# Performance work log

Measured on AMD Instinct MI355X. Metric: run time of the kernel, lower is better.

## Reference

```python
import jax, jax.numpy as jnp
import numpy as np
from jax import lax

D_MODEL = 1024
D_STATE = 16
EXPAND = 2
KERNEL = 4
BATCH = 4
SEQ = 4096
LN_EPS = 1e-5


def _ln(x, w, b):
    m = jnp.mean(x, axis=-1, keepdims=True)
    v = jnp.mean((x - m) ** 2, axis=-1, keepdims=True)
    return (x - m) * lax.rsqrt(v + LN_EPS) * w + b


def setup_inputs() -> dict:
    key = jax.random.key(0)
    ks = jax.random.split(key, 16)
    d, n, e, k = D_MODEL, D_STATE, EXPAND, KERNEL

    def lin(key, fan_in, shape):
        bound = 1.0 / np.sqrt(fan_in)
        return jax.random.uniform(key, shape, jnp.float32, -bound, bound)

    return {
        "x": jax.random.normal(ks[0], (BATCH, SEQ, d), jnp.float32),
        "ln1_w": jnp.ones((d,), jnp.float32),
        "ln1_b": jnp.zeros((d,), jnp.float32),
        "conv_w": lin(ks[1], k, (d, 1, k)),  # depthwise conv, groups=d -> fan_in=k
        "conv_b": lin(ks[2], k, (d,)),
        "lns_w": jnp.ones((d,), jnp.float32),
        "lns_b": jnp.zeros((d,), jnp.float32),
        "in_w": lin(ks[3], d, (d, 2 * d)),
        "in_b": lin(ks[4], d, (2 * d,)),
        "xp_w": lin(ks[5], d, (d, n)),
        "xp_b": lin(ks[6], d, (n,)),
        "A_log": jax.random.normal(ks[7], (n,), jnp.float32),
        "D": jax.random.normal(ks[8], (n, d), jnp.float32),
        "out_w": lin(ks[9], d, (d, d)),
        "out_b": lin(ks[10], d, (d,)),
        "ln2_w": jnp.ones((d,), jnp.float32),
        "ln2_b": jnp.zeros((d,), jnp.float32),
        "mlp_w1": lin(ks[11], d, (d, e * d)),
        "mlp_b1": lin(ks[12], d, (e * d,)),
        "mlp_w2": lin(ks[13], e * d, (e * d, d)),
        "mlp_b2": lin(ks[14], e * d, (d,)),
    }


def reference(x, ln1_w, ln1_b, conv_w, conv_b, lns_w, lns_b, in_w, in_b,
              xp_w, xp_b, A_log, D, out_w, out_b, ln2_w, ln2_b,
              mlp_w1, mlp_b1, mlp_w2, mlp_b2):
    b, s, d = x.shape
    # --- depthwise causal-padded conv branch (truncated to seq_len) ---
    xn = _ln(x, ln1_w, ln1_b)
    xc = jnp.transpose(xn, (0, 2, 1))  # (b, d, s)
    xc = lax.conv_general_dilated(
        xc, conv_w, window_strides=(1,), padding=[(KERNEL - 1, KERNEL - 1)],
        feature_group_count=d, dimension_numbers=("NCH", "OIH", "NCH"))
    xc = xc + conv_b[None, :, None]
    xc = jnp.transpose(xc, (0, 2, 1))[:, :s]  # (b, s, d)
    x = x + xc

    # --- SelectiveScanLayer ---
    residual = x
    xn = _ln(x, lns_w, lns_b)
    xz = xn @ in_w + in_b
    xp, z = jnp.split(xz, 2, axis=-1)
    xp = jax.nn.silu(xp)
    z = jax.nn.sigmoid(z)
    u = xp @ xp_w + xp_b  # (b, s, n)
    decay = jnp.exp(-jnp.exp(A_log))  # exp(A), A = -exp(A_log); (n,)

    u_t = jnp.transpose(u, (1, 0, 2))  # (s, b, n)

    def step(h, u_i):
        h = decay * h + u_i
        return h, h

    _, hs = lax.scan(step, jnp.zeros((b, D_STATE), x.dtype), u_t)  # (s, b, n)
    ys = jnp.einsum("sbn,nd->sbd", hs, D) * jnp.transpose(z, (1, 0, 2))
    ys = ys @ out_w + out_b  # (s, b, d)
    # faithful to original: torch stack gives (1,s,b,d), then .view(b,s,d)
    y = ys.reshape(b, s, d)
    x = residual + y

    # --- MLP (dropout inactive at eval) ---
    h = _ln(x, ln2_w, ln2_b)
    h = jax.nn.gelu(h @ mlp_w1 + mlp_b1, approximate=False)
    h = h @ mlp_w2 + mlp_b2
    return x + h
```

## Files before the change

### kernel.cpp

```cpp
#include <hip/hip_runtime.h>
#include <cstdint>
#include <cstddef>


typedef short bf16x8 __attribute__((ext_vector_type(8)));
typedef float f32x4 __attribute__((ext_vector_type(4)));

#define GLD16(gp, lp)                                                          \
  __builtin_amdgcn_global_load_lds(                                            \
      (__attribute__((address_space(1))) void*)(gp),                           \
      (__attribute__((address_space(3))) void*)(lp), 16, 0, 0)

static __device__ __forceinline__ ushort f2bf(float f) {
  union { float f; uint32_t u; } c; c.f = f;
  uint32_t r = c.u + 0x7FFFu + ((c.u >> 16) & 1u);
  return (ushort)(r >> 16);
}
static __device__ __forceinline__ float bf2f(ushort u) {
  union { uint32_t u; float f; } c; c.u = ((uint32_t)u) << 16;
  return c.f;
}

template <int BF16OUT>
__global__ __launch_bounds__(256) void ln_kernel(
    const float* __restrict__ x, const float* __restrict__ w,
    const float* __restrict__ b, void* __restrict__ out) {
  const int row = blockIdx.x;
  const int tid = threadIdx.x;
  const float4 v = ((const float4*)(x + (size_t)row * 1024))[tid];
  float s  = v.x + v.y + v.z + v.w;
  float s2 = v.x * v.x + v.y * v.y + v.z * v.z + v.w * v.w;
#pragma unroll
  for (int off = 32; off > 0; off >>= 1) {
    s  += __shfl_down(s, off);
    s2 += __shfl_down(s2, off);
  }
  __shared__ float red[8];
  const int wv = tid >> 6, ln = tid & 63;
  if (ln == 0) { red[wv] = s; red[4 + wv] = s2; }
  __syncthreads();
  s  = red[0] + red[1] + red[2] + red[3];
  s2 = red[4] + red[5] + red[6] + red[7];
  const float mean = s * (1.f / 1024.f);
  const float var  = s2 * (1.f / 1024.f) - mean * mean;
  const float rstd = rsqrtf(var + 1e-5f);
  const float4 wv4 = ((const float4*)w)[tid];
  const float4 bv4 = ((const float4*)b)[tid];
  const float o0 = (v.x - mean) * rstd * wv4.x + bv4.x;
  const float o1 = (v.y - mean) * rstd * wv4.y + bv4.y;
  const float o2 = (v.z - mean) * rstd * wv4.z + bv4.z;
  const float o3 = (v.w - mean) * rstd * wv4.w + bv4.w;
  if (BF16OUT) {
    ushort4 o; o.x = f2bf(o0); o.y = f2bf(o1); o.z = f2bf(o2); o.w = f2bf(o3);
    ((ushort4*)((ushort*)out + (size_t)row * 1024))[tid] = o;
  } else {
    float4 o; o.x = o0; o.y = o1; o.z = o2; o.w = o3;
    ((float4*)((float*)out + (size_t)row * 1024))[tid] = o;
  }
}

__global__ __launch_bounds__(256) void lnconv_kernel(
    const float* __restrict__ x, const float* __restrict__ ln1w,
    const float* __restrict__ ln1b, const float* __restrict__ cw,
    const float* __restrict__ cb, const float* __restrict__ lnsw,
    const float* __restrict__ lnsb, float* __restrict__ x1,
    ushort* __restrict__ abuf) {
  const int row = blockIdx.x;
  const int t = row & 4095;
  const int tid = threadIdx.x;
  const int wv = tid >> 6, ln = tid & 63;
  const float4* x4 = (const float4*)x;
  float4 xr[4];
  float s[4], q[4];
#pragma unroll
  for (int j = 0; j < 4; j++) {
    const int tt = t - 3 + j;
    if (tt >= 0)
      xr[j] = x4[(size_t)(row - 3 + j) * 256 + tid];
    else
      xr[j] = make_float4(0.f, 0.f, 0.f, 0.f);
    s[j] = xr[j].x + xr[j].y + xr[j].z + xr[j].w;
    q[j] = xr[j].x * xr[j].x + xr[j].y * xr[j].y + xr[j].z * xr[j].z +
           xr[j].w * xr[j].w;
  }
#pragma unroll
  for (int off = 32; off > 0; off >>= 1) {
#pragma unroll
    for (int j = 0; j < 4; j++) {
      s[j] += __shfl_down(s[j], off);
      q[j] += __shfl_down(q[j], off);
    }
  }
  __shared__ float red[4][8];
  __shared__ float red2[8];
  if (ln == 0) {
#pragma unroll
    for (int j = 0; j < 4; j++) { red[wv][j] = s[j]; red[wv][4 + j] = q[j]; }
  }
  __syncthreads();
  float4 wv4 = ((const float4*)ln1w)[tid];
  float4 bv4 = ((const float4*)ln1b)[tid];
  const int c0 = tid * 4;
  float4 acc = *(const float4*)(cb + c0);
  const float4 w0 = *(const float4*)(cw + (size_t)(c0 + 0) * 4);
  const float4 w1 = *(const float4*)(cw + (size_t)(c0 + 1) * 4);
  const float4 w2 = *(const float4*)(cw + (size_t)(c0 + 2) * 4);
  const float4 w3 = *(const float4*)(cw + (size_t)(c0 + 3) * 4);
#pragma unroll
  for (int j = 0; j < 4; j++) {
    if (t - 3 + j >= 0) {
      const float sm = red[0][j] + red[1][j] + red[2][j] + red[3][j];
      const float sq = red[0][4 + j] + red[1][4 + j] + red[2][4 + j] +
                       red[3][4 + j];
      const float mean = sm * (1.f / 1024.f);
      const float var  = sq * (1.f / 1024.f) - mean * mean;
      const float rstd = rsqrtf(var + 1e-5f);
      const float lx = (xr[j].x - mean) * rstd * wv4.x + bv4.x;
      const float ly = (xr[j].y - mean) * rstd * wv4.y + bv4.y;
      const float lz = (xr[j].z - mean) * rstd * wv4.z + bv4.z;
      const float lw = (xr[j].w - mean) * rstd * wv4.w + bv4.w;
      acc.x += lx * ((const float*)&w0)[j];
      acc.y += ly * ((const float*)&w1)[j];
      acc.z += lz * ((const float*)&w2)[j];
      acc.w += lw * ((const float*)&w3)[j];
    }
  }
  float4 o;
  o.x = xr[3].x + acc.x; o.y = xr[3].y + acc.y;
  o.z = xr[3].z + acc.z; o.w = xr[3].w + acc.w;
  ((float4*)x1)[(size_t)row * 256 + tid] = o;
  float s2 = o.x + o.y + o.z + o.w;
  float q2 = o.x * o.x + o.y * o.y + o.z * o.z + o.w * o.w;
#pragma unroll
  for (int off = 32; off > 0; off >>= 1) {
    s2 += __shfl_down(s2, off);
    q2 += __shfl_down(q2, off);
  }
  if (ln == 0) { red2[wv] = s2; red2[4 + wv] = q2; }
  __syncthreads();
  const float sm = red2[0] + red2[1] + red2[2] + red2[3];
  const float sq = red2[4] + red2[5] + red2[6] + red2[7];
  const float mean = sm * (1.f / 1024.f);
  const float var  = sq * (1.f / 1024.f) - mean * mean;
  const float rstd = rsqrtf(var + 1e-5f);
  wv4 = ((const float4*)lnsw)[tid];
  bv4 = ((const float4*)lnsb)[tid];
  ushort4 a;
  a.x = f2bf((o.x - mean) * rstd * wv4.x + bv4.x);
  a.y = f2bf((o.y - mean) * rstd * wv4.y + bv4.y);
  a.z = f2bf((o.z - mean) * rstd * wv4.z + bv4.z);
  a.w = f2bf((o.w - mean) * rstd * wv4.w + bv4.w);
  ((ushort4*)(abuf + (size_t)row * 1024))[tid] = a;
}

__global__ __launch_bounds__(256) void wt_all_kernel(
    const float* __restrict__ in_w, const float* __restrict__ out_w,
    const float* __restrict__ w1, const float* __restrict__ w2,
    ushort* __restrict__ in_wT, ushort* __restrict__ out_wT,
    ushort* __restrict__ w1T, ushort* __restrict__ w2T) {
  __shared__ float tile[32][33];
  const int idx = blockIdx.x;
  const float* src; ushort* dst; int K, N, n0, k0;
  if (idx < 2048) {
    src = in_w; dst = in_wT; K = 1024; N = 2048;
    n0 = (idx & 63) * 32; k0 = (idx >> 6) * 32;
  } else if (idx < 3072) {
    const int r = idx - 2048;
    src = out_w; dst = out_wT; K = 1024; N = 1024;
    n0 = (r & 31) * 32; k0 = (r >> 5) * 32;
  } else if (idx < 5120) {
    const int r = idx - 3072;
    src = w1; dst = w1T; K = 1024; N = 2048;
    n0 = (r & 63) * 32; k0 = (r >> 6) * 32;
  } else {
    const int r = idx - 5120;
    src = w2; dst = w2T; K = 2048; N = 1024;
    n0 = (r & 31) * 32; k0 = (r >> 5) * 32;
  }
  const int tx = threadIdx.x & 31, ty = threadIdx.x >> 5;
#pragma unroll
  for (int j = 0; j < 32; j += 8)
    tile[ty + j][tx] = src[(size_t)(k0 + ty + j) * N + n0 + tx];
  __syncthreads();
#pragma unroll
  for (int j = 0; j < 32; j += 8)
    dst[(size_t)(n0 + ty + j) * K + k0 + tx] = f2bf(tile[tx][ty + j]);
}

__global__ __launch_bounds__(256) void u_mfma_kernel(
    const ushort* __restrict__ xp, const float* __restrict__ xpw,
    const float* __restrict__ xpb, float* __restrict__ u) {
  __shared__ ushort Ws[16 * 1024];
  __shared__ ushort As[64 * 64];
  const int tid = threadIdx.x;
  const int wave = tid >> 6, lane = tid & 63;
  const int l16 = lane & 15, quad = lane >> 4;
  for (int e = tid; e < 16384; e += 256) {
    const int n = e & 15, k = e >> 4;
    Ws[n * 1024 + (((k >> 3) ^ (n & 7)) << 3) + (k & 7)] =
        f2bf(xpw[(size_t)k * 16 + n]);
  }
  const int bm0 = blockIdx.x * 64;
  const int srow = lane >> 3, sblk = (lane & 7) ^ (srow & 7);
  const ushort* Ag = xp + (size_t)(bm0 + wave * 16 + srow) * 1024 + sblk * 8;
  ushort* Al = &As[wave * 16 * 64];
  const int rsw = l16 & 7;
  f32x4 acc = (f32x4){0.f, 0.f, 0.f, 0.f};
  __syncthreads();
  for (int k0 = 0; k0 < 1024; k0 += 64) {
    GLD16(Ag + k0, Al);
    GLD16(Ag + k0 + (size_t)8 * 1024, Al + 512);
    __syncthreads();
#pragma unroll
    for (int kh = 0; kh < 2; kh++) {
      const bf16x8 aF = *(const bf16x8*)
          &As[(wave * 16 + l16) * 64 + (((kh * 4 + quad) ^ rsw) << 3)];
      const bf16x8 bF = *(const bf16x8*)
          &Ws[l16 * 1024 + ((((k0 >> 3) + kh * 4 + quad) ^ rsw) << 3)];
      acc = __builtin_amdgcn_mfma_f32_16x16x32_bf16(aF, bF, acc, 0, 0, 0);
    }
    __syncthreads();
  }
  const float bv = xpb[l16];
#pragma unroll
  for (int r = 0; r < 4; r++) {
    const int row = bm0 + wave * 16 + quad * 4 + r;
    u[(size_t)row * 16 + l16] = acc[r] + bv;
  }
}

__global__ __launch_bounds__(256) void scan_kernel(
    const float* __restrict__ u, const float* __restrict__ A_log,
    float* __restrict__ hs) {
  const int tid = threadIdx.x;
  const int b = blockIdx.x >> 4;
  const int n = blockIdx.x & 15;
  const float d = expf(-expf(A_log[n]));
  const int t0 = tid * 16;
  const float* up = u + ((size_t)b * 4096) * 16 + n;
  float loc[16];
  float h = 0.f;
#pragma unroll
  for (int i = 0; i < 16; i++) {
    h = d * h + up[(size_t)(t0 + i) * 16];
    loc[i] = h;
  }
  __shared__ float sv[256];
  sv[tid] = h;
  __syncthreads();
  float d16 = d * d; d16 *= d16; d16 *= d16; d16 *= d16;
  float f = d16;
  for (int off = 1; off < 256; off <<= 1) {
    const float add = (tid >= off) ? sv[tid - off] : 0.f;
    __syncthreads();
    sv[tid] += f * add;
    __syncthreads();
    f *= f;
  }
  const float carry = (tid > 0) ? sv[tid - 1] : 0.f;
  float dp = d;
#pragma unroll
  for (int i = 0; i < 16; i++) {
    const float hg = loc[i] + dp * carry;
    dp *= d;
    hs[((size_t)(t0 + i) * 4 + b) * 16 + n] = hg;
  }
}

__global__ __launch_bounds__(256) void g_kernel(
    const float* __restrict__ hs, const float* __restrict__ Dm,
    const ushort* __restrict__ z, ushort* __restrict__ g) {
  __shared__ float hsh[256];
  const int tid = threadIdx.x;
  const int r0 = blockIdx.x * 16;
  hsh[tid] = hs[(size_t)r0 * 16 + tid];
  __syncthreads();
  float4 acc[16];
#pragma unroll
  for (int rr = 0; rr < 16; rr++) acc[rr] = make_float4(0.f, 0.f, 0.f, 0.f);
  const float4* Dv = (const float4*)Dm;
#pragma unroll
  for (int n = 0; n < 16; n++) {
    const float4 dv = Dv[(size_t)n * 256 + tid];
#pragma unroll
    for (int rr = 0; rr < 16; rr++) {
      const float h = hsh[rr * 16 + n];
      acc[rr].x += h * dv.x; acc[rr].y += h * dv.y;
      acc[rr].z += h * dv.z; acc[rr].w += h * dv.w;
    }
  }
#pragma unroll
  for (int rr = 0; rr < 16; rr++) {
    const int r = r0 + rr;
    const int b = r & 3, t = r >> 2;
    const ushort4 zv =
        *(const ushort4*)(z + ((size_t)b * 4096 + t) * 1024 + tid * 4);
    ushort4 o;
    o.x = f2bf(acc[rr].x * bf2f(zv.x)); o.y = f2bf(acc[rr].y * bf2f(zv.y));
    o.z = f2bf(acc[rr].z * bf2f(zv.z)); o.w = f2bf(acc[rr].w * bf2f(zv.w));
    *(ushort4*)(g + (size_t)r * 1024 + tid * 4) = o;
  }
}

template <int EPI>
__global__ __launch_bounds__(512, 2) void gemm_bt(
    const ushort* __restrict__ A, const ushort* __restrict__ Bt,
    const float* __restrict__ bias, int K, void* __restrict__ p0,
    void* __restrict__ p1) {
  __shared__ __align__(16) ushort sm[65536];
  const int tid = threadIdx.x;
  const int wave = tid >> 6, lane = tid & 63;
  const int l16 = lane & 15, quad = lane >> 4;
  const int wm = wave >> 2, wn = wave & 3;

  const int nbx = (int)gridDim.x;
  int tm, tn;
  if ((nbx & 7) == 0) {
    const int lid = (int)blockIdx.y * nbx + (int)blockIdx.x;
    const int ncm = nbx >> 3;
    const int xcd = lid & 7;
    const int j = lid >> 3;
    tm = xcd * ncm + (j % ncm);
    tn = j / ncm;
  } else {
    tm = (int)blockIdx.x; tn = (int)blockIdx.y;
  }
  const int bm0 = tm * 256, bn0 = tn * 256;

  const int srow = lane >> 3;
  const int sblk = (lane & 7) ^ srow;
  const int NT = K >> 6;

  const ushort* Astg = A + (size_t)(bm0 + wave * 8 + srow) * K + sblk * 8;
  const ushort* Bstg = Bt + (size_t)(bn0 + wave * 8 + srow) * K + sblk * 8;

#define SA(i, kt, base)                                                        \
  GLD16(Astg + (size_t)((i) * 64) * K + (kt) * 64,                             \
        &sm[(base) + (i) * 4096 + wave * 512])
#define SB(i, kt, base)                                                        \
  GLD16(Bstg + (size_t)((i) * 64) * K + (kt) * 64,                             \
        &sm[(base) + 16384 + (i) * 4096 + wave * 512])

  const int rsw = l16 & 7;
  const int c80 = (quad ^ rsw) << 3;
  const int c81 = ((4 + quad) ^ rsw) << 3;
  const int aoff = (wm * 128 + l16) * 64;
  const int boff = 16384 + (wn * 64 + l16) * 64;

  f32x4 acc[8][4];
#pragma unroll
  for (int i = 0; i < 8; i++)
#pragma unroll
    for (int j = 0; j < 4; j++) acc[i][j] = (f32x4){0.f, 0.f, 0.f, 0.f};

  SA(0, 0, 0); SA(1, 0, 0); SA(2, 0, 0); SA(3, 0, 0);
  SB(0, 0, 0); SB(1, 0, 0); SB(2, 0, 0); SB(3, 0, 0);
  if (NT > 1) {
    SA(0, 1, 32768); SA(1, 1, 32768);
    asm volatile("s_waitcnt vmcnt(2)" ::: "memory");
  } else {
    asm volatile("s_waitcnt vmcnt(0)" ::: "memory");
  }
  __builtin_amdgcn_s_barrier();

  bf16x8 af[4][2], b01[2][2], b23[2][2];

  for (int t = 0; t < NT; ++t) {
    const int cb = (t & 1) << 15;
    const int nb = cb ^ 32768;
#pragma unroll
    for (int i = 0; i < 4; i++) {
      af[i][0] = *(const bf16x8*)&sm[cb + aoff + i * 1024 + c80];
      af[i][1] = *(const bf16x8*)&sm[cb + aoff + i * 1024 + c81];
    }
#pragma unroll
    for (int j = 0; j < 2; j++) {
      b01[j][0] = *(const bf16x8*)&sm[cb + boff + j * 1024 + c80];
      b01[j][1] = *(const bf16x8*)&sm[cb + boff + j * 1024 + c81];
    }
    if (t + 1 < NT) { SA(2, t + 1, nb); SA(3, t + 1, nb); }
    __builtin_amdgcn_s_barrier();
    asm volatile("s_waitcnt lgkmcnt(0)" ::: "memory");
    __builtin_amdgcn_sched_barrier(0);
    __builtin_amdgcn_s_setprio(1);
#pragma unroll
    for (int i = 0; i < 4; i++)
#pragma unroll
      for (int j = 0; j < 2; j++) {
        acc[i][j] = __builtin_amdgcn_mfma_f32_16x16x32_bf16(
            af[i][0], b01[j][0], acc[i][j], 0, 0, 0);
        acc[i][j] = __builtin_amdgcn_mfma_f32_16x16x32_bf16(
            af[i][1], b01[j][1], acc[i][j], 0, 0, 0);
      }
    __builtin_amdgcn_s_setprio(0);
    __builtin_amdgcn_s_barrier();
#pragma unroll
    for (int j = 0; j < 2; j++) {
      b23[j][0] = *(const bf16x8*)&sm[cb + boff + (2 + j) * 1024 + c80];
      b23[j][1] = *(const bf16x8*)&sm[cb + boff + (2 + j) * 1024 + c81];
    }
    if (t + 1 < NT) { SB(0, t + 1, nb); SB(1, t + 1, nb); }
    __builtin_amdgcn_s_barrier();
    asm volatile("s_waitcnt lgkmcnt(0)" ::: "memory");
    __builtin_amdgcn_sched_barrier(0);
    __builtin_amdgcn_s_setprio(1);
#pragma unroll
    for (int i = 0; i < 4; i++)
#pragma unroll
      for (int j = 0; j < 2; j++) {
        acc[i][2 + j] = __builtin_amdgcn_mfma_f32_16x16x32_bf16(
            af[i][0], b23[j][0], acc[i][2 + j], 0, 0, 0);
        acc[i][2 + j] = __builtin_amdgcn_mfma_f32_16x16x32_bf16(
            af[i][1], b23[j][1], acc[i][2 + j], 0, 0, 0);
      }
    __builtin_amdgcn_s_setprio(0);
    __builtin_amdgcn_s_barrier();
#pragma unroll
    for (int i = 0; i < 4; i++) {
      af[i][0] = *(const bf16x8*)&sm[cb + aoff + (4 + i) * 1024 + c80];
      af[i][1] = *(const bf16x8*)&sm[cb + aoff + (4 + i) * 1024 + c81];
    }
    if (t + 1 < NT) { SB(2, t + 1, nb); SB(3, t + 1, nb); }
    __builtin_amdgcn_s_barrier();
    asm volatile("s_waitcnt lgkmcnt(0)" ::: "memory");
    __builtin_amdgcn_sched_barrier(0);
    __builtin_amdgcn_s_setprio(1);
#pragma unroll
    for (int i = 0; i < 4; i++)
#pragma unroll
      for (int j = 0; j < 2; j++) {
        acc[4 + i][j] = __builtin_amdgcn_mfma_f32_16x16x32_bf16(
            af[i][0], b01[j][0], acc[4 + i][j], 0, 0, 0);
        acc[4 + i][j] = __builtin_amdgcn_mfma_f32_16x16x32_bf16(
            af[i][1], b01[j][1], acc[4 + i][j], 0, 0, 0);
      }
    __builtin_amdgcn_s_setprio(0);
    __builtin_amdgcn_s_barrier();
    if (t + 2 < NT) { SA(0, t + 2, cb); SA(1, t + 2, cb); }
    __builtin_amdgcn_s_barrier();
    __builtin_amdgcn_s_setprio(1);
#pragma unroll
    for (int i = 0; i < 4; i++)
#pragma unroll
      for (int j = 0; j < 2; j++) {
        acc[4 + i][2 + j] = __builtin_amdgcn_mfma_f32_16x16x32_bf16(
            af[i][0], b23[j][0], acc[4 + i][2 + j], 0, 0, 0);
        acc[4 + i][2 + j] = __builtin_amdgcn_mfma_f32_16x16x32_bf16(
            af[i][1], b23[j][1], acc[4 + i][2 + j], 0, 0, 0);
      }
    __builtin_amdgcn_s_setprio(0);
    if (t + 2 < NT) {
      asm volatile("s_waitcnt vmcnt(2)" ::: "memory");
    } else {
      asm volatile("s_waitcnt vmcnt(0)" ::: "memory");
    }
    __builtin_amdgcn_s_barrier();
  }
#undef SA
#undef SB

#pragma unroll
  for (int i = 0; i < 8; i++) {
    const int row0 = bm0 + wm * 128 + i * 16 + quad * 4;
#pragma unroll
    for (int j = 0; j < 4; j++) {
      const int c = bn0 + wn * 64 + j * 16 + l16;
      const float bv = bias[c];
#pragma unroll
      for (int r = 0; r < 4; r++) {
        const size_t row = (size_t)(row0 + r);
        const float v = acc[i][j][r] + bv;
        if (EPI == 0) {
          if (c < 1024)
            ((ushort*)p0)[row * 1024 + c] = f2bf(v / (1.f + __expf(-v)));
          else
            ((ushort*)p1)[row * 1024 + (c - 1024)] =
                f2bf(1.f / (1.f + __expf(-v)));
        } else if (EPI == 1) {
          float* io = (float*)p0;
          io[row * 1024 + c] += v;
        } else if (EPI == 2) {
          ((ushort*)p0)[row * 2048 + c] =
              f2bf(0.5f * v * (1.f + erff(v * 0.70710678118654752f)));
        } else {
          ((float*)p0)[row * 1024 + c] =
              ((const float*)p1)[row * 1024 + c] + v;
        }
      }
    }
  }
}

extern "C" void kernel_launch(void* const* d_in, const int* in_sizes, int n_in,
                              void* d_out, int out_size, void* d_ws,
                              size_t ws_size, hipStream_t stream) {
  const float* x      = (const float*)d_in[0];
  const float* ln1_w  = (const float*)d_in[1];
  const float* ln1_b  = (const float*)d_in[2];
  const float* conv_w = (const float*)d_in[3];
  const float* conv_b = (const float*)d_in[4];
  const float* lns_w  = (const float*)d_in[5];
  const float* lns_b  = (const float*)d_in[6];
  const float* in_w   = (const float*)d_in[7];
  const float* in_b   = (const float*)d_in[8];
  const float* xp_w   = (const float*)d_in[9];
  const float* xp_b   = (const float*)d_in[10];
  const float* A_log  = (const float*)d_in[11];
  const float* Dm     = (const float*)d_in[12];
  const float* out_w  = (const float*)d_in[13];
  const float* out_b  = (const float*)d_in[14];
  const float* ln2_w  = (const float*)d_in[15];
  const float* ln2_b  = (const float*)d_in[16];
  const float* mlp_w1 = (const float*)d_in[17];
  const float* mlp_b1 = (const float*)d_in[18];
  const float* mlp_w2 = (const float*)d_in[19];
  const float* mlp_b2 = (const float*)d_in[20];

  char* wsp = (char*)d_ws;
  size_t off = 0;
  auto alloc = [&](size_t bytes) {
    void* p = wsp + off;
    off += (bytes + 255) & ~(size_t)255;
    return p;
  };
  float*  x1    = (float*)alloc(67108864);
  ushort* abuf  = (ushort*)alloc(67108864);
  ushort* gbuf  = abuf + 16777216;
  ushort* xpb   = (ushort*)alloc(33554432);
  ushort* zb    = (ushort*)alloc(67108864);
  ushort* h1b   = (ushort*)zb;
  float*  ub    = (float*)alloc(1048576);
  float*  hsb   = (float*)alloc(1048576);
  ushort* in_wT = (ushort*)alloc(4194304);
  ushort* out_wT= (ushort*)alloc(2097152);
  ushort* w1T   = (ushort*)alloc(4194304);
  ushort* w2T   = (ushort*)alloc(4194304);

  wt_all_kernel<<<7168, 256, 0, stream>>>(in_w, out_w, mlp_w1, mlp_w2,
                                          in_wT, out_wT, w1T, w2T);
  lnconv_kernel<<<16384, 256, 0, stream>>>(x, ln1_w, ln1_b, conv_w, conv_b,
                                           lns_w, lns_b, x1, abuf);
  gemm_bt<0><<<dim3(64, 8), 512, 0, stream>>>(abuf, in_wT, in_b, 1024,
                                              xpb, zb);
  u_mfma_kernel<<<256, 256, 0, stream>>>(xpb, xp_w, xp_b, ub);
  scan_kernel<<<64, 256, 0, stream>>>(ub, A_log, hsb);
  g_kernel<<<1024, 256, 0, stream>>>(hsb, Dm, zb, gbuf);
  gemm_bt<1><<<dim3(64, 4), 512, 0, stream>>>(gbuf, out_wT, out_b, 1024,
                                              x1, nullptr);
  ln_kernel<1><<<16384, 256, 0, stream>>>(x1, ln2_w, ln2_b, xpb);
  gemm_bt<2><<<dim3(64, 8), 512, 0, stream>>>(xpb, w1T, mlp_b1, 1024,
                                              h1b, nullptr);
  gemm_bt<3><<<dim3(64, 4), 512, 0, stream>>>(h1b, w2T, mlp_b2, 2048,
                                              d_out, x1);
}
```

Measured before the change: 618.9 us.

## Prefetch whole next tiles up front and vectorize GEMM epilogue via transposed MFMA

The GEMM main loop no longer interleaves partial prefetches of the next K-tile between compute phases. It now issues all A and B loads for tile t+2 in one batch and waits with vmcnt(8), and one barrier is removed. The MFMA operand order is swapped so each lane holds four consecutive output columns. That lets the epilogue use float4 bias loads and 4-wide bf16 or float stores instead of scalar strided stores. The risk is that clustered loads cut overlap with compute and put more pressure on the double buffer's timing.

```diff
diff --git a/kernel.cpp b/kernel.cpp
--- a/kernel.cpp
+++ b/kernel.cpp
@@ -353,11 +353,12 @@
 #pragma unroll
     for (int j = 0; j < 4; j++) acc[i][j] = (f32x4){0.f, 0.f, 0.f, 0.f};
 
-  SA(0, 0, 0); SA(1, 0, 0); SA(2, 0, 0); SA(3, 0, 0);
-  SB(0, 0, 0); SB(1, 0, 0); SB(2, 0, 0); SB(3, 0, 0);
+#pragma unroll
+  for (int i = 0; i < 4; i++) { SA(i, 0, 0); SB(i, 0, 0); }
   if (NT > 1) {
-    SA(0, 1, 32768); SA(1, 1, 32768);
-    asm volatile("s_waitcnt vmcnt(2)" ::: "memory");
+#pragma unroll
+    for (int i = 0; i < 4; i++) { SA(i, 1, 32768); SB(i, 1, 32768); }
+    asm volatile("s_waitcnt vmcnt(8)" ::: "memory");
   } else {
     asm volatile("s_waitcnt vmcnt(0)" ::: "memory");
   }
@@ -367,7 +368,6 @@
 
   for (int t = 0; t < NT; ++t) {
     const int cb = (t & 1) << 15;
-    const int nb = cb ^ 32768;
 #pragma unroll
     for (int i = 0; i < 4; i++) {
       af[i][0] = *(const bf16x8*)&sm[cb + aoff + i * 1024 + c80];
@@ -378,7 +378,6 @@
       b01[j][0] = *(const bf16x8*)&sm[cb + boff + j * 1024 + c80];
       b01[j][1] = *(const bf16x8*)&sm[cb + boff + j * 1024 + c81];
     }
-    if (t + 1 < NT) { SA(2, t + 1, nb); SA(3, t + 1, nb); }
     __builtin_amdgcn_s_barrier();
     asm volatile("s_waitcnt lgkmcnt(0)" ::: "memory");
     __builtin_amdgcn_sched_barrier(0);
@@ -388,9 +387,9 @@
 #pragma unroll
       for (int j = 0; j < 2; j++) {
         acc[i][j] = __builtin_amdgcn_mfma_f32_16x16x32_bf16(
-            af[i][0], b01[j][0], acc[i][j], 0, 0, 0);
+            b01[j][0], af[i][0], acc[i][j], 0, 0, 0);
         acc[i][j] = __builtin_amdgcn_mfma_f32_16x16x32_bf16(
-            af[i][1], b01[j][1], acc[i][j], 0, 0, 0);
+            b01[j][1], af[i][1], acc[i][j], 0, 0, 0);
       }
     __builtin_amdgcn_s_setprio(0);
     __builtin_amdgcn_s_barrier();
@@ -399,7 +398,6 @@
       b23[j][0] = *(const bf16x8*)&sm[cb + boff + (2 + j) * 1024 + c80];
       b23[j][1] = *(const bf16x8*)&sm[cb + boff + (2 + j) * 1024 + c81];
     }
-    if (t + 1 < NT) { SB(0, t + 1, nb); SB(1, t + 1, nb); }
     __builtin_amdgcn_s_barrier();
     asm volatile("s_waitcnt lgkmcnt(0)" ::: "memory");
     __builtin_amdgcn_sched_barrier(0);
@@ -409,9 +407,9 @@
 #pragma unroll
       for (int j = 0; j < 2; j++) {
         acc[i][2 + j] = __builtin_amdgcn_mfma_f32_16x16x32_bf16(
-            af[i][0], b23[j][0], acc[i][2 + j], 0, 0, 0);
+            b23[j][0], af[i][0], acc[i][2 + j], 0, 0, 0);
         acc[i][2 + j] = __builtin_amdgcn_mfma_f32_16x16x32_bf16(
-            af[i][1], b23[j][1], acc[i][2 + j], 0, 0, 0);
+            b23[j][1], af[i][1], acc[i][2 + j], 0, 0, 0);
       }
     __builtin_amdgcn_s_setprio(0);
     __builtin_amdgcn_s_barrier();
@@ -420,7 +418,6 @@
       af[i][0] = *(const bf16x8*)&sm[cb + aoff + (4 + i) * 1024 + c80];
       af[i][1] = *(const bf16x8*)&sm[cb + aoff + (4 + i) * 1024 + c81];
     }
-    if (t + 1 < NT) { SB(2, t + 1, nb); SB(3, t + 1, nb); }
     __builtin_amdgcn_s_barrier();
     asm volatile("s_waitcnt lgkmcnt(0)" ::: "memory");
     __builtin_amdgcn_sched_barrier(0);
@@ -430,27 +427,29 @@
 #pragma unroll
       for (int j = 0; j < 2; j++) {
         acc[4 + i][j] = __builtin_amdgcn_mfma_f32_16x16x32_bf16(
-            af[i][0], b01[j][0], acc[4 + i][j], 0, 0, 0);
+            b01[j][0], af[i][0], acc[4 + i][j], 0, 0, 0);
         acc[4 + i][j] = __builtin_amdgcn_mfma_f32_16x16x32_bf16(
-            af[i][1], b01[j][1], acc[4 + i][j], 0, 0, 0);
+            b01[j][1], af[i][1], acc[4 + i][j], 0, 0, 0);
       }
     __builtin_amdgcn_s_setprio(0);
     __builtin_amdgcn_s_barrier();
-    if (t + 2 < NT) { SA(0, t + 2, cb); SA(1, t + 2, cb); }
-    __builtin_amdgcn_s_barrier();
+    if (t + 2 < NT) {
+#pragma unroll
+      for (int i = 0; i < 4; i++) { SA(i, t + 2, cb); SB(i, t + 2, cb); }
+    }
     __builtin_amdgcn_s_setprio(1);
 #pragma unroll
     for (int i = 0; i < 4; i++)
 #pragma unroll
       for (int j = 0; j < 2; j++) {
         acc[4 + i][2 + j] = __builtin_amdgcn_mfma_f32_16x16x32_bf16(
-            af[i][0], b23[j][0], acc[4 + i][2 + j], 0, 0, 0);
+            b23[j][0], af[i][0], acc[4 + i][2 + j], 0, 0, 0);
         acc[4 + i][2 + j] = __builtin_amdgcn_mfma_f32_16x16x32_bf16(
-            af[i][1], b23[j][1], acc[4 + i][2 + j], 0, 0, 0);
+            b23[j][1], af[i][1], acc[4 + i][2 + j], 0, 0, 0);
       }
     __builtin_amdgcn_s_setprio(0);
     if (t + 2 < NT) {
-      asm volatile("s_waitcnt vmcnt(2)" ::: "memory");
+      asm volatile("s_waitcnt vmcnt(8)" ::: "memory");
     } else {
       asm volatile("s_waitcnt vmcnt(0)" ::: "memory");
     }
@@ -461,31 +460,48 @@
 
 #pragma unroll
   for (int i = 0; i < 8; i++) {
-    const int row0 = bm0 + wm * 128 + i * 16 + quad * 4;
+    const size_t row = (size_t)(bm0 + wm * 128 + i * 16 + l16);
 #pragma unroll
     for (int j = 0; j < 4; j++) {
-      const int c = bn0 + wn * 64 + j * 16 + l16;
-      const float bv = bias[c];
-#pragma unroll
-      for (int r = 0; r < 4; r++) {
-        const size_t row = (size_t)(row0 + r);
-        const float v = acc[i][j][r] + bv;
-        if (EPI == 0) {
-          if (c < 1024)
-            ((ushort*)p0)[row * 1024 + c] = f2bf(v / (1.f + __expf(-v)));
-          else
-            ((ushort*)p1)[row * 1024 + (c - 1024)] =
-                f2bf(1.f / (1.f + __expf(-v)));
-        } else if (EPI == 1) {
-          float* io = (float*)p0;
-          io[row * 1024 + c] += v;
-        } else if (EPI == 2) {
-          ((ushort*)p0)[row * 2048 + c] =
-              f2bf(0.5f * v * (1.f + erff(v * 0.70710678118654752f)));
+      const int c = bn0 + wn * 64 + j * 16 + quad * 4;
+      const float4 bv = *(const float4*)(bias + c);
+      const float v0 = acc[i][j][0] + bv.x;
+      const float v1 = acc[i][j][1] + bv.y;
+      const float v2 = acc[i][j][2] + bv.z;
+      const float v3 = acc[i][j][3] + bv.w;
+      if (EPI == 0) {
+        ushort4 o;
+        if (c < 1024) {
+          o.x = f2bf(v0 / (1.f + __expf(-v0)));
+          o.y = f2bf(v1 / (1.f + __expf(-v1)));
+          o.z = f2bf(v2 / (1.f + __expf(-v2)));
+          o.w = f2bf(v3 / (1.f + __expf(-v3)));
+          *(ushort4*)((ushort*)p0 + row * 1024 + c) = o;
         } else {
-          ((float*)p0)[row * 1024 + c] =
-              ((const float*)p1)[row * 1024 + c] + v;
+          o.x = f2bf(1.f / (1.f + __expf(-v0)));
+          o.y = f2bf(1.f / (1.f + __expf(-v1)));
+          o.z = f2bf(1.f / (1.f + __expf(-v2)));
+          o.w = f2bf(1.f / (1.f + __expf(-v3)));
+          *(ushort4*)((ushort*)p1 + row * 1024 + (c - 1024)) = o;
         }
+      } else if (EPI == 1) {
+        float4* io = (float4*)((float*)p0 + row * 1024 + c);
+        float4 t4 = *io;
+        t4.x += v0; t4.y += v1; t4.z += v2; t4.w += v3;
+        *io = t4;
+      } else if (EPI == 2) {
+        ushort4 o;
+        o.x = f2bf(0.5f * v0 * (1.f + erff(v0 * 0.70710678118654752f)));
+        o.y = f2bf(0.5f * v1 * (1.f + erff(v1 * 0.70710678118654752f)));
+        o.z = f2bf(0.5f * v2 * (1.f + erff(v2 * 0.70710678118654752f)));
+        o.w = f2bf(0.5f * v3 * (1.f + erff(v3 * 0.70710678118654752f)));
+        *(ushort4*)((ushort*)p0 + row * 2048 + c) = o;
+      } else {
+        const float4 pv = *(const float4*)((const float*)p1 + row * 1024 + c);
+        float4 t4;
+        t4.x = pv.x + v0; t4.y = pv.y + v1;
+        t4.z = pv.z + v2; t4.w = pv.w + v3;
+        *(float4*)((float*)p0 + row * 1024 + c) = t4;
       }
     }
   }
```

Result: slower. 636.9 us (+2.9%).
